# Kernel optimization log

Measured on AMD Instinct MI355X. Metric: run time of the kernel, lower is better.

Reference implementation:

```python
import jax, jax.numpy as jnp
import numpy as np

B, X, Y, Z, C = 1, 16, 16, 16, 768
NUM_HEADS = 12


def setup_inputs() -> dict:
    key = jax.random.key(0)
    k0, k1, k2 = jax.random.split(key, 3)
    x = jax.random.normal(k0, (B, X, Y, Z, C), dtype=jnp.float32)
    # Linear weights stored as [in, out] (torch stores [out, in]; math is x @ W_in_out + b)
    w_qkv = jax.random.normal(k1, (C, 3 * C), dtype=jnp.float32) * 0.02
    b_qkv = jnp.zeros((3 * C,), dtype=jnp.float32)
    w_proj = jax.random.normal(k2, (C, C), dtype=jnp.float32) * 0.02
    b_proj = jnp.zeros((C,), dtype=jnp.float32)
    return {"x": x, "w_qkv": w_qkv, "b_qkv": b_qkv, "w_proj": w_proj, "b_proj": b_proj}


def reference(x, w_qkv, b_qkv, w_proj, b_proj):
    b, xx, yy, zz, c = x.shape
    h = NUM_HEADS
    hd = c // h
    scale = hd ** (-0.5)
    n = xx * yy * zz  # flatten 3D grid into tokens

    qkv = x.reshape(b, n, c) @ w_qkv + b_qkv          # [B, N, 3C]
    qkv = qkv.reshape(b, n, 3, h, hd).transpose(2, 0, 3, 1, 4)  # [3, B, H, N, hd]
    q, k, v = qkv[0], qkv[1], qkv[2]

    attn = jnp.einsum('bhnd,bhmd->bhnm', q * scale, k)  # [B, H, N, N]
    attn = jax.nn.softmax(attn, axis=-1)
    out = jnp.einsum('bhnm,bhmd->bhnd', attn, v)        # [B, H, N, hd]
    out = out.transpose(0, 2, 1, 3).reshape(b, n, c)
    out = out @ w_proj + b_proj
    return out.reshape(b, xx, yy, zz, c)
```

## Files before the change

### kernel.cpp

```cpp
#include <hip/hip_runtime.h>
#include <cstddef>

#define N_TOK 4096
#define C_DIM 768
#define H_NUM 12
#define C3    2304
#define NSPL  4

typedef unsigned short u16;
using short8  = __attribute__((ext_vector_type(8))) short;
using floatx4 = __attribute__((ext_vector_type(4))) float;
using u16x4   = __attribute__((ext_vector_type(4))) u16;
using uint2v  = __attribute__((ext_vector_type(2))) unsigned;

#define K2SCALE 0.18033688011112043f

__device__ __forceinline__ u16 f2bf(float f) {
  union { float f; unsigned u; } v; v.f = f;
  unsigned r = v.u + 0x7FFFu + ((v.u >> 16) & 1u);
  return (u16)(r >> 16);
}

__device__ __forceinline__ unsigned permpack(float a, float b) {
  union { float f; unsigned u; } x, y; x.f = a; y.f = b;
  return __builtin_amdgcn_perm(y.u, x.u, 0x07060302u);
}

__device__ __forceinline__ float aexp2(float x) {
  float r;
  asm("v_exp_f32 %0, %1" : "=v"(r) : "v"(x));
  return r;
}

__device__ __forceinline__ float arcp(float x) {
  float r;
  asm("v_rcp_f32 %0, %1" : "=v"(r) : "v"(x));
  return r;
}

__device__ __forceinline__ void gload_lds16(const void* g, void* l) {
  __builtin_amdgcn_global_load_lds(
      (const __attribute__((address_space(1))) unsigned int*)g,
      (__attribute__((address_space(3))) unsigned int*)l, 16, 0, 0);
}

__global__ void k_pre(const float* __restrict__ x, u16* __restrict__ xb,
                      const float* __restrict__ wq, u16* __restrict__ wqT,
                      const float* __restrict__ wp, u16* __restrict__ wpT) {
  __shared__ float tile[32][33];
  const int b = blockIdx.x;
  if (b < 3072) {
    int i = b * 256 + threadIdx.x;
    float4 f = ((const float4*)x)[i];
    u16x4 o;
    o[0] = f2bf(f.x); o[1] = f2bf(f.y); o[2] = f2bf(f.z); o[3] = f2bf(f.w);
    ((u16x4*)xb)[i] = o;
    return;
  }
  const float* in; u16* out; int Cc, bx, by;
  if (b < 4800) { int t = b - 3072; in = wq; out = wqT; Cc = 2304; bx = t % 72; by = t / 72; }
  else          { int t = b - 4800; in = wp; out = wpT; Cc = 768;  bx = t % 24; by = t / 24; }
  const int R = 768;
  const int tx = threadIdx.x & 31;
  const int ty = threadIdx.x >> 5;
  const int c0 = bx * 32, r0 = by * 32;
#pragma unroll
  for (int i = 0; i < 32; i += 8)
    tile[ty + i][tx] = in[(size_t)(r0 + ty + i) * Cc + c0 + tx];
  __syncthreads();
#pragma unroll
  for (int i = 0; i < 32; i += 8)
    out[(size_t)(c0 + ty + i) * R + r0 + tx] = f2bf(tile[tx][ty + i]);
}

template <int MODE>
__global__ __launch_bounds__(256)
void k_gemm_bt(const u16* __restrict__ A, const u16* __restrict__ B,
               const float* __restrict__ bias, void* __restrict__ outp,
               u16* __restrict__ vT, int K) {
  __shared__ u16 As[128 * 32];
  __shared__ u16 Bs[128 * 32];
  const int tid  = threadIdx.x;
  const int wave = tid >> 6, lane = tid & 63, quad = lane >> 4, l16 = lane & 15;
  const int wrow = wave >> 1, wcol = wave & 1;
  const int bm = blockIdx.y, bn = blockIdx.x;
  const int r3 = l16 & 3;

  floatx4 acc[4][4];
#pragma unroll
  for (int i = 0; i < 4; ++i)
#pragma unroll
    for (int j = 0; j < 4; ++j)
#pragma unroll
      for (int r = 0; r < 4; ++r) acc[i][j][r] = 0.f;

  const int ar = tid >> 2;
  const int ac = ((tid & 3) ^ (ar & 3)) * 8;
  const u16* gA = A + (size_t)(bm * 128 + ar) * K + ac;
  const u16* gB = B + (size_t)(bn * 128 + ar) * K + ac;
  u16* lA = &As[0] + tid * 8;
  u16* lB = &Bs[0] + tid * 8;

  for (int k0 = 0; k0 < K; k0 += 32) {
    gload_lds16(gA + k0,                  lA);
    gload_lds16(gA + k0 + (size_t)64 * K, lA + 2048);
    gload_lds16(gB + k0,                  lB);
    gload_lds16(gB + k0 + (size_t)64 * K, lB + 2048);
    __syncthreads();
    short8 af[4], bf[4];
#pragma unroll
    for (int t = 0; t < 4; ++t) {
      af[t] = *(const short8*)&As[(wrow * 64 + t * 16 + l16) * 32 + ((quad ^ r3) * 8)];
      bf[t] = *(const short8*)&Bs[(wcol * 64 + t * 16 + l16) * 32 + ((quad ^ r3) * 8)];
    }
#pragma unroll
    for (int tm = 0; tm < 4; ++tm)
#pragma unroll
      for (int tn = 0; tn < 4; ++tn)
        acc[tm][tn] = __builtin_amdgcn_mfma_f32_16x16x32_bf16(af[tm], bf[tn], acc[tm][tn], 0, 0, 0);
    __syncthreads();
  }

  if (MODE == 0) {
    u16* qkv = (u16*)outp;
    const float qs = (bn < 6) ? K2SCALE : 1.0f;
#pragma unroll
    for (int tn = 0; tn < 4; ++tn) {
      const int col = bn * 128 + wcol * 64 + tn * 16 + l16;
      const float bc = bias[col];
      if (col < 1536) {
#pragma unroll
        for (int tm = 0; tm < 4; ++tm) {
          const int rowb = bm * 128 + wrow * 64 + tm * 16 + quad * 4;
#pragma unroll
          for (int r = 0; r < 4; ++r)
            qkv[(size_t)(rowb + r) * C3 + col] = f2bf((acc[tm][tn][r] + bc) * qs);
        }
      } else {
        const int hd_ = col - 1536;
#pragma unroll
        for (int tm = 0; tm < 4; ++tm) {
          const int rowb = bm * 128 + wrow * 64 + tm * 16 + quad * 4;
          u16x4 pk;
#pragma unroll
          for (int r = 0; r < 4; ++r) pk[r] = f2bf(acc[tm][tn][r] + bc);
          *(u16x4*)&vT[(size_t)hd_ * N_TOK + rowb] = pk;
        }
      }
    }
  } else {
    float* out = (float*)outp;
#pragma unroll
    for (int tn = 0; tn < 4; ++tn) {
      const int col = bn * 128 + wcol * 64 + tn * 16 + l16;
      const float bc = bias[col];
#pragma unroll
      for (int tm = 0; tm < 4; ++tm) {
        const int rowb = bm * 128 + wrow * 64 + tm * 16 + quad * 4;
#pragma unroll
        for (int r = 0; r < 4; ++r)
          out[(size_t)(rowb + r) * C_DIM + col] = acc[tm][tn][r] + bc;
      }
    }
  }
}

__global__ __launch_bounds__(256)
void k_flash(const u16* __restrict__ qkv, const u16* __restrict__ vT,
             float* __restrict__ Opart, float* __restrict__ lpart) {
  __shared__ u16 Ks[2][64 * 64];
  __shared__ u16 Vs[2][64 * 64];
  __shared__ u16 Ps[4][64 * 32];
  const int tid  = threadIdx.x;
  const int wave = tid >> 6, lane = tid & 63, quad = lane >> 4, l16 = lane & 15;
  const int qt = blockIdx.x, h = blockIdx.y, split = blockIdx.z;
  const int lr = tid >> 3;
  const int lc = ((tid & 7) ^ (lr & 7)) * 8;
  const int r7 = l16 & 7;
  const int r3 = l16 & 3;
  const int kb = split * (N_TOK / NSPL);
  const int nt = (N_TOK / NSPL) / 64;

  short8 bq[4][2];
#pragma unroll
  for (int qs = 0; qs < 4; ++qs)
#pragma unroll
    for (int dh = 0; dh < 2; ++dh)
      bq[qs][dh] = *(const short8*)&qkv[(size_t)(qt * 256 + wave * 64 + qs * 16 + l16) * C3
                                        + h * 64 + dh * 32 + quad * 8];

  const u16* gk = qkv + (size_t)lr * C3 + C_DIM + h * 64 + lc;
  const u16* gv = vT + (size_t)(h * 64 + lr) * N_TOK + lc;

  auto stage = [&](int b, int m0) {
#pragma unroll
    for (int p = 0; p < 2; ++p) {
      gload_lds16(gk + (size_t)(m0 + p * 32) * C3,    &Ks[b][p * 2048 + tid * 8]);
      gload_lds16(gv + (size_t)(p * 32) * N_TOK + m0, &Vs[b][p * 2048 + tid * 8]);
    }
  };

  floatx4 o[4][4], l[4], zv;
#pragma unroll
  for (int r = 0; r < 4; ++r) zv[r] = 0.f;
#pragma unroll
  for (int qs = 0; qs < 4; ++qs) {
#pragma unroll
    for (int r = 0; r < 4; ++r) l[qs][r] = 0.f;
#pragma unroll
    for (int dt = 0; dt < 4; ++dt)
#pragma unroll
      for (int r = 0; r < 4; ++r) o[qs][dt][r] = 0.f;
  }

  short8 ones;
#pragma unroll
  for (int i = 0; i < 8; ++i) ones[i] = (short)0x3F80;

  u16* psw = &Ps[wave][0];

  auto compute = [&](int b) __attribute__((always_inline)) {
    const u16* kbp = &Ks[b][0];
    const u16* vb  = &Vs[b][0];
#pragma unroll
    for (int kh = 0; kh < 2; ++kh) {
      short8 ak[2][2];
#pragma unroll
      for (int tl = 0; tl < 2; ++tl)
#pragma unroll
        for (int dh = 0; dh < 2; ++dh)
          ak[tl][dh] = *(const short8*)&kbp[((kh * 2 + tl) * 16 + l16) * 64
                                            + ((dh * 4 + quad) ^ r7) * 8];
#pragma unroll
      for (int qs = 0; qs < 4; ++qs) {
        floatx4 s0 = __builtin_amdgcn_mfma_f32_16x16x32_bf16(ak[0][0], bq[qs][0], zv, 0, 0, 0);
        floatx4 s1 = __builtin_amdgcn_mfma_f32_16x16x32_bf16(ak[1][0], bq[qs][0], zv, 0, 0, 0);
        s0 = __builtin_amdgcn_mfma_f32_16x16x32_bf16(ak[0][1], bq[qs][1], s0, 0, 0, 0);
        s1 = __builtin_amdgcn_mfma_f32_16x16x32_bf16(ak[1][1], bq[qs][1], s1, 0, 0, 0);
        const int row = qs * 16 + l16;
        unsigned pa0 = permpack(aexp2(s0[0]), aexp2(s0[1]));
        unsigned pa1 = permpack(aexp2(s0[2]), aexp2(s0[3]));
        unsigned pb0 = permpack(aexp2(s1[0]), aexp2(s1[1]));
        unsigned pb1 = permpack(aexp2(s1[2]), aexp2(s1[3]));
        uint2v w0; w0[0] = pa0; w0[1] = pa1;
        uint2v w1; w1[0] = pb0; w1[1] = pb1;
        *(uint2v*)&psw[row * 32 + (((quad >> 1)) ^ r3) * 8 + (quad & 1) * 4]     = w0;
        *(uint2v*)&psw[row * 32 + ((2 + (quad >> 1)) ^ r3) * 8 + (quad & 1) * 4] = w1;
      }
      short8 ap[4];
#pragma unroll
      for (int qs = 0; qs < 4; ++qs)
        ap[qs] = *(const short8*)&psw[(qs * 16 + l16) * 32 + ((quad ^ r3) * 8)];
#pragma unroll
      for (int dt = 0; dt < 4; ++dt) {
        short8 bv = *(const short8*)&vb[(dt * 16 + l16) * 64 + ((kh * 4 + quad) ^ r7) * 8];
#pragma unroll
        for (int qs = 0; qs < 4; ++qs)
          o[qs][dt] = __builtin_amdgcn_mfma_f32_16x16x32_bf16(ap[qs], bv, o[qs][dt], 0, 0, 0);
      }
#pragma unroll
      for (int qs = 0; qs < 4; ++qs)
        l[qs] = __builtin_amdgcn_mfma_f32_16x16x32_bf16(ap[qs], ones, l[qs], 0, 0, 0);
    }
  };

  stage(0, kb);
  __syncthreads();
  int m0 = kb + 64;
  for (int t = 1; t < nt; ++t) {
    stage(t & 1, m0);
    m0 += 64;
    compute((t - 1) & 1);
    __syncthreads();
  }
  compute((nt - 1) & 1);

  float* Ob = Opart + ((size_t)(split * H_NUM + h) * N_TOK) * 64;
  float* lb = lpart + (size_t)(split * H_NUM + h) * N_TOK;
#pragma unroll
  for (int qs = 0; qs < 4; ++qs) {
    const int rowg = qt * 256 + wave * 64 + qs * 16 + quad * 4;
#pragma unroll
    for (int r = 0; r < 4; ++r) {
#pragma unroll
      for (int dt = 0; dt < 4; ++dt)
        Ob[(size_t)(rowg + r) * 64 + dt * 16 + l16] = o[qs][dt][r];
      if (l16 == 0) lb[rowg + r] = l[qs][r];
    }
  }
}

__global__ void k_combine(const float* __restrict__ Op, const float* __restrict__ lp,
                          u16* __restrict__ ao) {
  const int idx = blockIdx.x * 256 + threadIdx.x;
  const int col = idx & 63;
  const int row = idx >> 6;
  float o = 0.f, l = 0.f;
#pragma unroll
  for (int s = 0; s < NSPL; ++s) {
    o += Op[((size_t)row + (size_t)s * H_NUM * N_TOK) * 64 + col];
    l += lp[row + s * H_NUM * N_TOK];
  }
  const int h = row >> 12, q = row & 4095;
  ao[(size_t)q * C_DIM + h * 64 + col] = f2bf(o * arcp(l));
}

extern "C" void kernel_launch(void* const* d_in, const int* in_sizes, int n_in,
                              void* d_out, int out_size, void* d_ws, size_t ws_size,
                              hipStream_t stream) {
  const float* x      = (const float*)d_in[0];
  const float* w_qkv  = (const float*)d_in[1];
  const float* b_qkv  = (const float*)d_in[2];
  const float* w_proj = (const float*)d_in[3];
  const float* b_proj = (const float*)d_in[4];
  float* out = (float*)d_out;

  u16* xb     = (u16*)d_ws;
  u16* wqkvT  = xb     + (size_t)N_TOK * C_DIM;
  u16* wprojT = wqkvT  + (size_t)C3 * C_DIM;
  u16* qkv    = wprojT + (size_t)C_DIM * C_DIM;
  u16* vT     = qkv    + (size_t)N_TOK * C3;
  u16* ao     = vT     + (size_t)C_DIM * N_TOK;
  float* Opart = (float*)(ao + (size_t)N_TOK * C_DIM);
  float* lpart = Opart + (size_t)NSPL * H_NUM * N_TOK * 64;

  k_pre<<<5376, 256, 0, stream>>>(x, xb, w_qkv, wqkvT, w_proj, wprojT);
  k_gemm_bt<0><<<dim3(C3 / 128, N_TOK / 128), 256, 0, stream>>>(xb, wqkvT, b_qkv, qkv, vT, C_DIM);
  k_flash<<<dim3(N_TOK / 256, H_NUM, NSPL), 256, 0, stream>>>(qkv, vT, Opart, lpart);
  k_combine<<<H_NUM * N_TOK * 64 / 256, 256, 0, stream>>>(Opart, lpart, ao);
  k_gemm_bt<1><<<dim3(C_DIM / 128, N_TOK / 128), 256, 0, stream>>>(ao, wprojT, b_proj, out, nullptr, C_DIM);
}
```

Before: 218.7 us.

## Use single-wave flash blocks without LDS sharing and halve key splits

Rewrites the attention kernel to launch one 64-thread wave per block, handling 64 queries with a single-buffered K/V tile staged directly and synchronised by waitcnt instead of block barriers. The key-dimension split count is halved to 2, which reduces partial-output traffic and combine work. This removes __syncthreads and cross-wave coupling, but K/V tiles are no longer shared across four waves, which raises global/L2 load traffic. With a single buffer, load latency is no longer overlapped with compute within a block and must be hidden by occupancy.

```diff
diff --git a/kernel.cpp b/kernel.cpp
--- a/kernel.cpp
+++ b/kernel.cpp
@@ -5,7 +5,7 @@
 #define C_DIM 768
 #define H_NUM 12
 #define C3    2304
-#define NSPL  4
+#define NSPL  2
 
 typedef unsigned short u16;
 using short8  = __attribute__((ext_vector_type(8))) short;
@@ -165,40 +165,31 @@
   }
 }
 
-__global__ __launch_bounds__(256)
+__global__ __launch_bounds__(64)
 void k_flash(const u16* __restrict__ qkv, const u16* __restrict__ vT,
              float* __restrict__ Opart, float* __restrict__ lpart) {
-  __shared__ u16 Ks[2][64 * 64];
-  __shared__ u16 Vs[2][64 * 64];
-  __shared__ u16 Ps[4][64 * 32];
+  __shared__ u16 Ks[64 * 64];
+  __shared__ u16 Vs[64 * 64];
+  __shared__ u16 Ps[64 * 32];
   const int tid  = threadIdx.x;
-  const int wave = tid >> 6, lane = tid & 63, quad = lane >> 4, l16 = lane & 15;
+  const int quad = tid >> 4, l16 = tid & 15;
   const int qt = blockIdx.x, h = blockIdx.y, split = blockIdx.z;
-  const int lr = tid >> 3;
-  const int lc = ((tid & 7) ^ (lr & 7)) * 8;
-  const int r7 = l16 & 7;
-  const int r3 = l16 & 3;
+  const int r7 = l16 & 7, r3 = l16 & 3;
   const int kb = split * (N_TOK / NSPL);
-  const int nt = (N_TOK / NSPL) / 64;
+
+  const int sr  = tid >> 3;
+  const int lc8 = ((tid & 7) ^ (sr & 7)) * 8;
 
   short8 bq[4][2];
 #pragma unroll
   for (int qs = 0; qs < 4; ++qs)
 #pragma unroll
     for (int dh = 0; dh < 2; ++dh)
-      bq[qs][dh] = *(const short8*)&qkv[(size_t)(qt * 256 + wave * 64 + qs * 16 + l16) * C3
+      bq[qs][dh] = *(const short8*)&qkv[(size_t)(qt * 64 + qs * 16 + l16) * C3
                                         + h * 64 + dh * 32 + quad * 8];
 
-  const u16* gk = qkv + (size_t)lr * C3 + C_DIM + h * 64 + lc;
-  const u16* gv = vT + (size_t)(h * 64 + lr) * N_TOK + lc;
-
-  auto stage = [&](int b, int m0) {
-#pragma unroll
-    for (int p = 0; p < 2; ++p) {
-      gload_lds16(gk + (size_t)(m0 + p * 32) * C3,    &Ks[b][p * 2048 + tid * 8]);
-      gload_lds16(gv + (size_t)(p * 32) * N_TOK + m0, &Vs[b][p * 2048 + tid * 8]);
-    }
-  };
+  const u16* gk0 = qkv + (size_t)sr * C3 + C_DIM + h * 64 + lc8;
+  const u16* gv0 = vT + (size_t)(h * 64 + sr) * N_TOK + lc8;
 
   floatx4 o[4][4], l[4], zv;
 #pragma unroll
@@ -217,11 +208,17 @@
 #pragma unroll
   for (int i = 0; i < 8; ++i) ones[i] = (short)0x3F80;
 
-  u16* psw = &Ps[wave][0];
-
-  auto compute = [&](int b) __attribute__((always_inline)) {
-    const u16* kbp = &Ks[b][0];
-    const u16* vb  = &Vs[b][0];
+  int m0 = kb;
+  for (int t = 0; t < (N_TOK / NSPL) / 64; ++t) {
+    asm volatile("s_waitcnt lgkmcnt(0)" ::: "memory");
+#pragma unroll
+    for (int i = 0; i < 8; ++i) {
+      gload_lds16(gk0 + (size_t)(m0 + i * 8) * C3,    &Ks[i * 512 + tid * 8]);
+      gload_lds16(gv0 + (size_t)(i * 8) * N_TOK + m0, &Vs[i * 512 + tid * 8]);
+    }
+    m0 += 64;
+    asm volatile("s_waitcnt vmcnt(0)" ::: "memory");
+
 #pragma unroll
     for (int kh = 0; kh < 2; ++kh) {
       short8 ak[2][2];
@@ -229,8 +226,8 @@
       for (int tl = 0; tl < 2; ++tl)
 #pragma unroll
         for (int dh = 0; dh < 2; ++dh)
-          ak[tl][dh] = *(const short8*)&kbp[((kh * 2 + tl) * 16 + l16) * 64
-                                            + ((dh * 4 + quad) ^ r7) * 8];
+          ak[tl][dh] = *(const short8*)&Ks[((kh * 2 + tl) * 16 + l16) * 64
+                                           + ((dh * 4 + quad) ^ r7) * 8];
 #pragma unroll
       for (int qs = 0; qs < 4; ++qs) {
         floatx4 s0 = __builtin_amdgcn_mfma_f32_16x16x32_bf16(ak[0][0], bq[qs][0], zv, 0, 0, 0);
@@ -244,16 +241,16 @@
         unsigned pb1 = permpack(aexp2(s1[2]), aexp2(s1[3]));
         uint2v w0; w0[0] = pa0; w0[1] = pa1;
         uint2v w1; w1[0] = pb0; w1[1] = pb1;
-        *(uint2v*)&psw[row * 32 + (((quad >> 1)) ^ r3) * 8 + (quad & 1) * 4]     = w0;
-        *(uint2v*)&psw[row * 32 + ((2 + (quad >> 1)) ^ r3) * 8 + (quad & 1) * 4] = w1;
+        *(uint2v*)&Ps[row * 32 + (((quad >> 1)) ^ r3) * 8 + (quad & 1) * 4]     = w0;
+        *(uint2v*)&Ps[row * 32 + ((2 + (quad >> 1)) ^ r3) * 8 + (quad & 1) * 4] = w1;
       }
       short8 ap[4];
 #pragma unroll
       for (int qs = 0; qs < 4; ++qs)
-        ap[qs] = *(const short8*)&psw[(qs * 16 + l16) * 32 + ((quad ^ r3) * 8)];
+        ap[qs] = *(const short8*)&Ps[(qs * 16 + l16) * 32 + ((quad ^ r3) * 8)];
 #pragma unroll
       for (int dt = 0; dt < 4; ++dt) {
-        short8 bv = *(const short8*)&vb[(dt * 16 + l16) * 64 + ((kh * 4 + quad) ^ r7) * 8];
+        short8 bv = *(const short8*)&Vs[(dt * 16 + l16) * 64 + ((kh * 4 + quad) ^ r7) * 8];
 #pragma unroll
         for (int qs = 0; qs < 4; ++qs)
           o[qs][dt] = __builtin_amdgcn_mfma_f32_16x16x32_bf16(ap[qs], bv, o[qs][dt], 0, 0, 0);
@@ -262,24 +259,13 @@
       for (int qs = 0; qs < 4; ++qs)
         l[qs] = __builtin_amdgcn_mfma_f32_16x16x32_bf16(ap[qs], ones, l[qs], 0, 0, 0);
     }
-  };
-
-  stage(0, kb);
-  __syncthreads();
-  int m0 = kb + 64;
-  for (int t = 1; t < nt; ++t) {
-    stage(t & 1, m0);
-    m0 += 64;
-    compute((t - 1) & 1);
-    __syncthreads();
-  }
-  compute((nt - 1) & 1);
+  }
 
   float* Ob = Opart + ((size_t)(split * H_NUM + h) * N_TOK) * 64;
   float* lb = lpart + (size_t)(split * H_NUM + h) * N_TOK;
 #pragma unroll
   for (int qs = 0; qs < 4; ++qs) {
-    const int rowg = qt * 256 + wave * 64 + qs * 16 + quad * 4;
+    const int rowg = qt * 64 + qs * 16 + quad * 4;
 #pragma unroll
     for (int r = 0; r < 4; ++r) {
 #pragma unroll
@@ -326,7 +312,7 @@
 
   k_pre<<<5376, 256, 0, stream>>>(x, xb, w_qkv, wqkvT, w_proj, wprojT);
   k_gemm_bt<0><<<dim3(C3 / 128, N_TOK / 128), 256, 0, stream>>>(xb, wqkvT, b_qkv, qkv, vT, C_DIM);
-  k_flash<<<dim3(N_TOK / 256, H_NUM, NSPL), 256, 0, stream>>>(qkv, vT, Opart, lpart);
+  k_flash<<<dim3(N_TOK / 64, H_NUM, NSPL), 64, 0, stream>>>(qkv, vT, Opart, lpart);
   k_combine<<<H_NUM * N_TOK * 64 / 256, 256, 0, stream>>>(Opart, lpart, ao);
   k_gemm_bt<1><<<dim3(C_DIM / 128, N_TOK / 128), 256, 0, stream>>>(ao, wprojT, b_proj, out, nullptr, C_DIM);
 }
```

New measurement: 248.4 us. 13.6% more time.
